# Kernel tuning notes

Hardware: AMD Instinct MI355X
Metric: run time of the kernel (lower is better)

## Reference

```python
import jax, jax.numpy as jnp
import numpy as np

B, N = 2, 200
IMG = 2048
NC = 4                    # node concepts ('Is*')
NODE_CH = NC * 256        # 1024
EC = 3                    # edge concepts minus 'HigherPri'
AC = 4                    # actions
BBOX_MAX = 1024.0
E = N * (N - 1)

# static fully-connected directed edge list (src=i, dst=j, i!=j), row-major order
_ii, _jj = np.meshgrid(np.arange(N), np.arange(N), indexing='ij')
_m = _ii != _jj
SRC = jnp.asarray(_ii[_m])
DST = jnp.asarray(_jj[_m])


def _lin(k, fin, fout):
    kw, kb = jax.random.split(k)
    s = 1.0 / np.sqrt(fin)
    return (jax.random.uniform(kw, (fin, fout), jnp.float32, -s, s),
            jax.random.uniform(kb, (fout,), jnp.float32, -s, s))


def setup_inputs():
    ks = jax.random.split(jax.random.key(0), 16)
    p = {}
    p['roi_features'] = jax.random.normal(ks[0], (B, N, IMG), jnp.float32)
    p['batch_bboxes'] = jax.random.uniform(ks[1], (B, N, 4), jnp.float32) * BBOX_MAX
    p['batch_directions'] = jax.random.normal(ks[2], (B, N, 4), jnp.float32)
    p['batch_priorities'] = jax.random.normal(ks[3], (B, N), jnp.float32)
    p['w1'], p['b1'] = _lin(ks[4], IMG, 512)
    p['w2'], p['b2'] = _lin(ks[5], 512, 256)
    p['w3'], p['b3'] = _lin(ks[6], 256, NODE_CH)
    p['wi'], p['bi'] = _lin(ks[7], NODE_CH, NC)
    p['we1'], p['be1'] = _lin(ks[8], 16, 256)
    p['we2'], p['be2'] = _lin(ks[9], 256, 64)
    p['we3'], p['be3'] = _lin(ks[10], 64, EC)
    p['wp1'], p['bp1'] = _lin(ks[11], EC + 1, 128)
    p['wp2'], p['bp2'] = _lin(ks[12], 128, NODE_CH * AC)
    p['root_w'], _ = _lin(ks[13], NODE_CH, AC)
    _, p['root_b'] = _lin(ks[14], NODE_CH, AC)
    return p


def reference(roi_features, batch_bboxes, batch_directions, batch_priorities,
              w1, b1, w2, b2, w3, b3, wi, bi,
              we1, be1, we2, be2, we3, be3,
              wp1, bp1, wp2, bp2, root_w, root_b):
    # node concept embedding MLP: [B,N,IMG] -> [B,N,NODE_CH]
    h = jax.nn.relu(roi_features @ w1 + b1)
    h = jax.nn.relu(h @ w2 + b2)
    node_concepts = h @ w3 + b3
    node_concepts_explicit = jax.nn.sigmoid(node_concepts @ wi + bi)

    # pairwise attributes for all directed edges (same ordering as torch masks)
    node_attr = jnp.concatenate([batch_bboxes / BBOX_MAX, batch_directions], -1)  # [B,N,8]
    pair = jnp.concatenate([node_attr[:, SRC], node_attr[:, DST]], -1)            # [B,E,16]
    eh = jax.nn.relu(pair @ we1 + be1)
    eh = jax.nn.relu(eh @ we2 + be2)
    edge_attributes = jax.nn.sigmoid(eh @ we3 + be3)                              # [B,E,EC]
    higher_pri = (batch_priorities[:, SRC] > batch_priorities[:, DST]).astype(jnp.float32)
    edge_attributes = jnp.concatenate([edge_attributes, higher_pri[..., None]], -1)  # [B,E,EC+1]

    # NNConv on graph 0: per-edge weight matrix, gather-matmul-scatter
    x = node_concepts[0]                 # [N, NODE_CH]
    e = edge_attributes[0]               # [E, EC+1]
    w = jax.nn.relu(e @ wp1 + bp1) @ wp2 + bp2
    w = w.reshape(E, NODE_CH, AC)        # [E, NODE_CH, AC]
    msg = jnp.einsum('ei,eio->eo', x[SRC], w)          # [E, AC]
    agg = jax.ops.segment_sum(msg, DST, num_segments=N)  # [N, AC]
    next_actions = agg + x @ root_w + root_b
    return (next_actions, node_concepts_explicit[0], edge_attributes[0])
```

## Files before the change

kernel.cpp:

```cpp
#include <hip/hip_runtime.h>
#include <math.h>

#define NN 200
#define ETOT 39800

typedef float float4v __attribute__((ext_vector_type(4)));
typedef short short8 __attribute__((ext_vector_type(8)));
typedef unsigned int uint4v __attribute__((ext_vector_type(4)));

__device__ __forceinline__ float sigf(float x) { return 1.0f / (1.0f + expf(-x)); }

__device__ __forceinline__ unsigned short f2b(float f) {
  unsigned u = __float_as_uint(f);
  u += 0x7fffu + ((u >> 16) & 1u);
  return (unsigned short)(u >> 16);
}
__device__ __forceinline__ float b2f16(unsigned short u) {
  return __uint_as_float(((unsigned)u) << 16);
}
__device__ __forceinline__ unsigned pkbf(float a, float b) {
  return (unsigned)f2b(a) | ((unsigned)f2b(b) << 16);
}

__global__ __launch_bounds__(256) void k_prep(
    const float* __restrict__ w1, const float* __restrict__ w2, const float* __restrict__ w3,
    const float* __restrict__ wp2, const float* __restrict__ we2,
    const float* __restrict__ bbox, const float* __restrict__ dir,
    const float* __restrict__ we1, const float* __restrict__ be1,
    const float* __restrict__ roi, const float* __restrict__ wp1,
    unsigned short* __restrict__ w1T, unsigned short* __restrict__ w2T,
    unsigned short* __restrict__ w3T, unsigned short* __restrict__ WrT,
    unsigned short* __restrict__ we2T, unsigned short* __restrict__ roiB,
    float* __restrict__ P, float* __restrict__ Q, float* __restrict__ wp1T) {
  __shared__ float lds[64][65];
  const int b = blockIdx.x, tid = threadIdx.x;

  if (b < 352) {
    const float* Wf;
    unsigned short* Wt;
    int K, N, t;
    if (b < 256) { Wf = w1; Wt = w1T; K = 2048; N = 512; t = b; }
    else if (b < 288) { Wf = w2; Wt = w2T; K = 512; N = 256; t = b - 256; }
    else { Wf = w3; Wt = w3T; K = 256; N = 1024; t = b - 288; }
    const int K64 = K >> 6;
    const int kt = t % K64, nt = t / K64;
#pragma unroll 4
    for (int i = 0; i < 16; ++i) {
      int idx = tid + i * 256;
      int r = idx >> 6, c = idx & 63;
      lds[r][c] = Wf[(size_t)(kt * 64 + r) * N + nt * 64 + c];
    }
    __syncthreads();
#pragma unroll 4
    for (int i = 0; i < 16; ++i) {
      int idx = tid + i * 256;
      int r = idx >> 6, c = idx & 63;
      Wt[(size_t)(nt * 64 + r) * K + kt * 64 + c] = f2b(lds[c][r]);
    }
  } else if (b < 480) {
    int k = b - 352;
    int o = tid >> 6, l = tid & 63;
    const float* src = wp2 + (size_t)k * 4096;
    unsigned short* dst = WrT + (size_t)(k * 4 + o) * 1024;
    for (int i = l; i < 1024; i += 64) dst[i] = f2b(src[i * 4 + o]);
  } else if (b < 496) {
    int f = (b - 480) * 256 + tid;
    int c = f >> 6, k0 = (f & 63) * 4;
#pragma unroll
    for (int q = 0; q < 4; ++q)
      we2T[c * 256 + k0 + q] = f2b(we2[(k0 + q) * 64 + c]);
  } else if (b < 696) {
    int n = b - 496, c = tid;
    float a[8];
#pragma unroll
    for (int r = 0; r < 4; ++r) a[r] = bbox[n * 4 + r] * (1.0f / 1024.0f);
#pragma unroll
    for (int r = 0; r < 4; ++r) a[4 + r] = dir[n * 4 + r];
    float p = be1[c], q = 0.0f;
#pragma unroll
    for (int r = 0; r < 8; ++r) {
      p += a[r] * we1[r * 256 + c];
      q += a[r] * we1[(8 + r) * 256 + c];
    }
    P[n * 256 + c] = p;
    Q[n * 256 + c] = q;
  } else if (b < 896) {
    int n = b - 696;
    const float4v* R4 = (const float4v*)(roi + (size_t)n * 2048);
    unsigned long long* O = (unsigned long long*)(roiB + (size_t)n * 2048);
#pragma unroll
    for (int j = 0; j < 2; ++j) {
      int idx = tid + j * 256;
      float4v v = R4[idx];
      union { unsigned short us[4]; unsigned long long ll; } pk;
#pragma unroll
      for (int q = 0; q < 4; ++q) pk.us[q] = f2b(v[q]);
      O[idx] = pk.ll;
    }
  } else {
    if (tid < 128) {
      float4v v = {wp1[tid], wp1[128 + tid], wp1[256 + tid], wp1[384 + tid]};
      ((float4v*)wp1T)[tid] = v;
    }
  }
}

template <int KSTEPS, int RELU, int OUTF32, int HASBIAS>
__global__ __launch_bounds__(256) void gemm_mf(const unsigned short* __restrict__ A,
                                               const unsigned short* __restrict__ B,
                                               const float* __restrict__ bias,
                                               void* __restrict__ Cout, int N) {
  constexpr int K = KSTEPS * 128;
  const int tid = threadIdx.x, lane = tid & 63, wv = tid >> 6;
  const int m0 = blockIdx.x * 16, n0 = blockIdx.y * 16;
  const int mr = lane & 15, quad = lane >> 4;
  const unsigned short* Ap = A + (size_t)(m0 + mr) * K + wv * (KSTEPS * 32) + quad * 8;
  const unsigned short* Bp = B + (size_t)(n0 + mr) * K + wv * (KSTEPS * 32) + quad * 8;
  float4v acc = {0.f, 0.f, 0.f, 0.f};
#pragma unroll
  for (int s = 0; s < KSTEPS; ++s) {
    short8 af = *(const short8*)(Ap + s * 32);
    short8 bf = *(const short8*)(Bp + s * 32);
    acc = __builtin_amdgcn_mfma_f32_16x16x32_bf16(af, bf, acc, 0, 0, 0);
  }
  __shared__ float red[4][16][17];
#pragma unroll
  for (int r = 0; r < 4; ++r) red[wv][quad * 4 + r][mr] = acc[r];
  __syncthreads();
  const int row = tid >> 4, col = tid & 15;
  float v = red[0][row][col] + red[1][row][col] + red[2][row][col] + red[3][row][col];
  if (HASBIAS) v += bias[n0 + col];
  if (RELU) v = fmaxf(v, 0.f);
  if (OUTF32)
    ((float*)Cout)[(size_t)(m0 + row) * N + n0 + col] = v;
  else
    ((unsigned short*)Cout)[(size_t)(m0 + row) * N + n0 + col] = f2b(v);
}

__global__ __launch_bounds__(256) void k_nodevec(const unsigned short* __restrict__ xB,
                                                 const float* __restrict__ wi, const float* __restrict__ bi,
                                                 const float* __restrict__ root_w, const float* __restrict__ root_b,
                                                 const float* __restrict__ bp2,
                                                 float* __restrict__ out_nce, float* __restrict__ U,
                                                 float* __restrict__ out0) {
  const int n = blockIdx.x, tid = threadIdx.x;
  float s[12] = {};
#pragma unroll
  for (int i = 0; i < 4; ++i) {
    int k = tid + i * 256;
    float xv = b2f16(xB[n * 1024 + k]);
    float4v wi4 = ((const float4v*)wi)[k];
    float4v rw4 = ((const float4v*)root_w)[k];
    float4v bp4 = ((const float4v*)bp2)[k];
#pragma unroll
    for (int c = 0; c < 4; ++c) {
      s[c] += xv * wi4[c];
      s[4 + c] += xv * rw4[c];
      s[8 + c] += xv * bp4[c];
    }
  }
  __shared__ float part[4][12];
  const int lane = tid & 63, wv = tid >> 6;
#pragma unroll
  for (int r = 0; r < 12; ++r) {
    float v = s[r];
#pragma unroll
    for (int off = 32; off > 0; off >>= 1) v += __shfl_down(v, off, 64);
    if (lane == 0) part[wv][r] = v;
  }
  __syncthreads();
  if (tid < 12) {
    float v = part[0][tid] + part[1][tid] + part[2][tid] + part[3][tid];
    int kind = tid >> 2, c = tid & 3;
    if (kind == 0) out_nce[n * 4 + c] = sigf(v + bi[c]);
    else if (kind == 1) out0[n * 4 + c] = v + root_b[c];
    else U[n * 4 + c] = v;
  }
}

__global__ __launch_bounds__(256) void k_edge(
    const float* __restrict__ P, const float* __restrict__ Q,
    const unsigned short* __restrict__ we2T,
    const float* __restrict__ be2, const float* __restrict__ we3, const float* __restrict__ be3,
    const float* __restrict__ wp1T, const float* __restrict__ bp1,
    const float* __restrict__ pri,
    const float* __restrict__ T, const float* __restrict__ U,
    float* __restrict__ out0, float* __restrict__ out_ea) {
  __shared__ int src_s[64], dst_s[64];
  __shared__ float ea_s[64][4];
  __shared__ float4v wp1s[128];
  __shared__ float bp1s[128];
  __shared__ float4v Ts[2][128];
  __shared__ float Us[2][4];

  const int tid = threadIdx.x;
  const int e0 = blockIdx.x * 64;
  const int s_lo = e0 / 199;

  if (tid < 64) {
    int e = e0 + tid;
    int i = -1, j = 0;
    if (e < ETOT) {
      i = e / 199;
      int jj = e - i * 199;
      j = jj + (jj >= i ? 1 : 0);
    }
    src_s[tid] = i;
    dst_s[tid] = j;
  }
  if (tid < 128) {
    wp1s[tid] = ((const float4v*)wp1T)[tid];
    bp1s[tid] = bp1[tid];
  }
  {
    int row = tid >> 7, c = tid & 127;
    Ts[row][c] = ((const float4v*)T)[(s_lo + row) * 128 + c];
  }
  if (tid < 8) {
    int s = min(s_lo + (tid >> 2), 199);
    Us[tid >> 2][tid & 3] = U[s * 4 + (tid & 3)];
  }
  __syncthreads();

  const int lane = tid & 63;
  const int wv = tid >> 6;
  const int m = lane & 15;
  const int quad = lane >> 4;
  const int eloc = wv * 16 + m;
  const int si = src_s[eloc];
  const int dj = dst_s[eloc];

  float4v acc[4];
#pragma unroll
  for (int ct = 0; ct < 4; ++ct) { acc[ct][0] = 0.f; acc[ct][1] = 0.f; acc[ct][2] = 0.f; acc[ct][3] = 0.f; }

  const short8* W8 = (const short8*)we2T;

  for (int ks = 0; ks < 8; ++ks) {
    union { short8 s; uint4v u; } af;
    af.s = (short8)0;
    if (si >= 0) {
      const float4v* p4 = (const float4v*)(P + si * 256 + ks * 32 + quad * 8);
      const float4v* q4 = (const float4v*)(Q + dj * 256 + ks * 32 + quad * 8);
      float4v v0 = p4[0] + q4[0];
      float4v v1 = p4[1] + q4[1];
      af.u[0] = pkbf(fmaxf(v0[0], 0.f), fmaxf(v0[1], 0.f));
      af.u[1] = pkbf(fmaxf(v0[2], 0.f), fmaxf(v0[3], 0.f));
      af.u[2] = pkbf(fmaxf(v1[0], 0.f), fmaxf(v1[1], 0.f));
      af.u[3] = pkbf(fmaxf(v1[2], 0.f), fmaxf(v1[3], 0.f));
    }
#pragma unroll
    for (int ct = 0; ct < 4; ++ct) {
      short8 bf = W8[(ct * 16 + m) * 32 + ks * 4 + quad];
      acc[ct] = __builtin_amdgcn_mfma_f32_16x16x32_bf16(af.s, bf, acc[ct], 0, 0, 0);
    }
  }

  float ev[4][3];
#pragma unroll
  for (int r = 0; r < 4; ++r) { ev[r][0] = 0.f; ev[r][1] = 0.f; ev[r][2] = 0.f; }
#pragma unroll
  for (int ct = 0; ct < 4; ++ct) {
    const int col = ct * 16 + m;
    const float b2v = be2[col];
    const float w0 = we3[col * 3 + 0], w1v = we3[col * 3 + 1], w2v = we3[col * 3 + 2];
#pragma unroll
    for (int r = 0; r < 4; ++r) {
      float e2 = fmaxf(acc[ct][r] + b2v, 0.f);
      ev[r][0] += e2 * w0;
      ev[r][1] += e2 * w1v;
      ev[r][2] += e2 * w2v;
    }
  }
#pragma unroll
  for (int r = 0; r < 4; ++r)
#pragma unroll
    for (int p = 0; p < 3; ++p) {
      float v = ev[r][p];
      v += __shfl_xor(v, 1, 64);
      v += __shfl_xor(v, 2, 64);
      v += __shfl_xor(v, 4, 64);
      v += __shfl_xor(v, 8, 64);
      ev[r][p] = v;
    }
  if (m == 0) {
#pragma unroll
    for (int r = 0; r < 4; ++r) {
      int el = wv * 16 + quad * 4 + r;
      int ss = src_s[el], dd = dst_s[el];
      if (ss >= 0) {
        float4v o;
        o[0] = sigf(ev[r][0] + be3[0]);
        o[1] = sigf(ev[r][1] + be3[1]);
        o[2] = sigf(ev[r][2] + be3[2]);
        o[3] = (pri[ss] > pri[dd]) ? 1.0f : 0.0f;
        *(float4v*)&ea_s[el][0] = o;
        *(float4v*)(out_ea + (size_t)(e0 + el) * 4) = o;
      }
    }
  }
  __syncthreads();

  const int ee = tid >> 2, pp = tid & 3;
  const int s2 = src_s[ee], d2 = dst_s[ee];
  float4v pm = {0.f, 0.f, 0.f, 0.f};
  if (s2 >= 0) {
    const int srow = s2 - s_lo;
    const float c0 = ea_s[ee][0], c1 = ea_s[ee][1], c2 = ea_s[ee][2], c3 = ea_s[ee][3];
#pragma unroll 8
    for (int t = pp; t < 128; t += 4) {
      float4v w4 = wp1s[t];
      float hv = bp1s[t] + c0 * w4[0] + c1 * w4[1] + c2 * w4[2] + c3 * w4[3];
      hv = fmaxf(hv, 0.f);
      pm += hv * Ts[srow][t];
    }
  }
#pragma unroll
  for (int o = 0; o < 4; ++o) {
    float v = pm[o];
    v += __shfl_xor(v, 1, 64);
    v += __shfl_xor(v, 2, 64);
    pm[o] = v;
  }
  if (s2 >= 0) atomicAdd(&out0[d2 * 4 + pp], Us[s2 - s_lo][pp] + pm[pp]);
}

extern "C" void kernel_launch(void* const* d_in, const int* in_sizes, int n_in,
                              void* d_out, int out_size, void* d_ws, size_t ws_size,
                              hipStream_t stream) {
  (void)in_sizes; (void)n_in; (void)out_size; (void)ws_size;
  const float* roi   = (const float*)d_in[0];
  const float* bbox  = (const float*)d_in[1];
  const float* dir   = (const float*)d_in[2];
  const float* pri   = (const float*)d_in[3];
  const float* w1    = (const float*)d_in[4];
  const float* b1    = (const float*)d_in[5];
  const float* w2    = (const float*)d_in[6];
  const float* b2    = (const float*)d_in[7];
  const float* w3    = (const float*)d_in[8];
  const float* b3    = (const float*)d_in[9];
  const float* wi    = (const float*)d_in[10];
  const float* bi    = (const float*)d_in[11];
  const float* we1   = (const float*)d_in[12];
  const float* be1   = (const float*)d_in[13];
  const float* we2   = (const float*)d_in[14];
  const float* be2   = (const float*)d_in[15];
  const float* we3   = (const float*)d_in[16];
  const float* be3   = (const float*)d_in[17];
  const float* wp1   = (const float*)d_in[18];
  const float* bp1   = (const float*)d_in[19];
  const float* wp2   = (const float*)d_in[20];
  const float* bp2   = (const float*)d_in[21];
  const float* rootw = (const float*)d_in[22];
  const float* rootb = (const float*)d_in[23];

  float* out0 = (float*)d_out;
  float* out1 = out0 + 800;
  float* out2 = out0 + 1600;

  unsigned short* us = (unsigned short*)d_ws;
  unsigned short* w1T  = us;
  unsigned short* w2T  = us + 1048576;
  unsigned short* w3T  = us + 1179648;
  unsigned short* WrT  = us + 1441792;
  unsigned short* we2T = us + 1966080;
  unsigned short* roiB = us + 1982464;
  unsigned short* h1   = us + 2408448;
  unsigned short* h2   = us + 2514944;
  unsigned short* xB   = us + 2568192;
  float* fb   = (float*)(us + 2781184);
  float* Tm   = fb;
  float* Pm   = fb + 106496;
  float* Qm   = fb + 157696;
  float* Um   = fb + 208896;
  float* wp1T = fb + 209696;

  k_prep<<<897, 256, 0, stream>>>(w1, w2, w3, wp2, we2, bbox, dir, we1, be1, roi, wp1,
                                  w1T, w2T, w3T, WrT, we2T, roiB, Pm, Qm, wp1T);

  gemm_mf<16, 1, 0, 1><<<dim3(13, 32), 256, 0, stream>>>(roiB, w1T, b1, h1, 512);
  gemm_mf<4, 1, 0, 1><<<dim3(13, 16), 256, 0, stream>>>(h1, w2T, b2, h2, 256);
  gemm_mf<2, 0, 0, 1><<<dim3(13, 64), 256, 0, stream>>>(h2, w3T, b3, xB, 1024);

  k_nodevec<<<200, 256, 0, stream>>>(xB, wi, bi, rootw, rootb, bp2, out1, Um, out0);

  gemm_mf<8, 0, 1, 0><<<dim3(13, 32), 256, 0, stream>>>(xB, WrT, nullptr, Tm, 512);

  k_edge<<<622, 256, 0, stream>>>(Pm, Qm, we2T, be2, we3, be3, wp1T, bp1, pri, Tm, Um, out0, out2);
}
```

Before: 157.2 us.

## Fuse GEMM chain, nodevec and edge kernels into persistent kernel with grid barriers

Replaces six separate kernel launches with one persistent 512-block kernel that loops over tiles for each stage and separates stages with atomic-counter grid barriers. It also runs the Wr GEMM and the node-vector reductions in the same phase. The aim is to remove per-launch overhead and the inter-kernel drain gaps. In exchange it relies on all 512 blocks being co-resident, or the barriers deadlock, and it adds barrier spin cost plus extra syncthreads inside each tile.

Result: slower. 600.8 us (+282.3%).

```diff
diff --git a/kernel.cpp b/kernel.cpp
--- a/kernel.cpp
+++ b/kernel.cpp
@@ -6,7 +6,6 @@
 
 typedef float float4v __attribute__((ext_vector_type(4)));
 typedef short short8 __attribute__((ext_vector_type(8)));
-typedef unsigned int uint4v __attribute__((ext_vector_type(4)));
 
 __device__ __forceinline__ float sigf(float x) { return 1.0f / (1.0f + expf(-x)); }
 
@@ -18,8 +17,18 @@
 __device__ __forceinline__ float b2f16(unsigned short u) {
   return __uint_as_float(((unsigned)u) << 16);
 }
-__device__ __forceinline__ unsigned pkbf(float a, float b) {
-  return (unsigned)f2b(a) | ((unsigned)f2b(b) << 16);
+
+__device__ __forceinline__ void gbar(unsigned* c, unsigned target) {
+  __threadfence();
+  __syncthreads();
+  if (threadIdx.x == 0) {
+    __hip_atomic_fetch_add(c, 1u, __ATOMIC_ACQ_REL, __HIP_MEMORY_SCOPE_AGENT);
+    while (__hip_atomic_load(c, __ATOMIC_ACQUIRE, __HIP_MEMORY_SCOPE_AGENT) < target) {
+      __builtin_amdgcn_s_sleep(2);
+    }
+  }
+  __syncthreads();
+  __threadfence();
 }
 
 __global__ __launch_bounds__(256) void k_prep(
@@ -31,7 +40,8 @@
     unsigned short* __restrict__ w1T, unsigned short* __restrict__ w2T,
     unsigned short* __restrict__ w3T, unsigned short* __restrict__ WrT,
     unsigned short* __restrict__ we2T, unsigned short* __restrict__ roiB,
-    float* __restrict__ P, float* __restrict__ Q, float* __restrict__ wp1T) {
+    float* __restrict__ P, float* __restrict__ Q, float* __restrict__ wp1T,
+    unsigned* __restrict__ barr) {
   __shared__ float lds[64][65];
   const int b = blockIdx.x, tid = threadIdx.x;
 
@@ -101,18 +111,23 @@
     if (tid < 128) {
       float4v v = {wp1[tid], wp1[128 + tid], wp1[256 + tid], wp1[384 + tid]};
       ((float4v*)wp1T)[tid] = v;
-    }
-  }
-}
+    } else if (tid < 136) {
+      barr[tid - 128] = 0u;
+    }
+  }
+}
+
 
 template <int KSTEPS, int RELU, int OUTF32, int HASBIAS>
-__global__ __launch_bounds__(256) void gemm_mf(const unsigned short* __restrict__ A,
-                                               const unsigned short* __restrict__ B,
-                                               const float* __restrict__ bias,
-                                               void* __restrict__ Cout, int N) {
+__device__ __forceinline__ void gemm_tile(char* sm, int t,
+                                          const unsigned short* __restrict__ A,
+                                          const unsigned short* __restrict__ B,
+                                          const float* __restrict__ bias,
+                                          void* __restrict__ Cout, int N) {
+  float (*red)[16][17] = (float (*)[16][17])sm;
   constexpr int K = KSTEPS * 128;
   const int tid = threadIdx.x, lane = tid & 63, wv = tid >> 6;
-  const int m0 = blockIdx.x * 16, n0 = blockIdx.y * 16;
+  const int m0 = (t % 13) * 16, n0 = (t / 13) * 16;
   const int mr = lane & 15, quad = lane >> 4;
   const unsigned short* Ap = A + (size_t)(m0 + mr) * K + wv * (KSTEPS * 32) + quad * 8;
   const unsigned short* Bp = B + (size_t)(n0 + mr) * K + wv * (KSTEPS * 32) + quad * 8;
@@ -123,7 +138,7 @@
     short8 bf = *(const short8*)(Bp + s * 32);
     acc = __builtin_amdgcn_mfma_f32_16x16x32_bf16(af, bf, acc, 0, 0, 0);
   }
-  __shared__ float red[4][16][17];
+  __syncthreads();
 #pragma unroll
   for (int r = 0; r < 4; ++r) red[wv][quad * 4 + r][mr] = acc[r];
   __syncthreads();
@@ -137,13 +152,15 @@
     ((unsigned short*)Cout)[(size_t)(m0 + row) * N + n0 + col] = f2b(v);
 }
 
-__global__ __launch_bounds__(256) void k_nodevec(const unsigned short* __restrict__ xB,
-                                                 const float* __restrict__ wi, const float* __restrict__ bi,
-                                                 const float* __restrict__ root_w, const float* __restrict__ root_b,
-                                                 const float* __restrict__ bp2,
-                                                 float* __restrict__ out_nce, float* __restrict__ U,
-                                                 float* __restrict__ out0) {
-  const int n = blockIdx.x, tid = threadIdx.x;
+__device__ __forceinline__ void nodevec_task(char* sm, int n,
+                                             const unsigned short* __restrict__ xB,
+                                             const float* __restrict__ wi, const float* __restrict__ bi,
+                                             const float* __restrict__ root_w, const float* __restrict__ root_b,
+                                             const float* __restrict__ bp2,
+                                             float* __restrict__ out_nce, float* __restrict__ U,
+                                             float* __restrict__ out0) {
+  float (*part)[12] = (float (*)[12])sm;
+  const int tid = threadIdx.x;
   float s[12] = {};
 #pragma unroll
   for (int i = 0; i < 4; ++i) {
@@ -159,8 +176,8 @@
       s[8 + c] += xv * bp4[c];
     }
   }
-  __shared__ float part[4][12];
   const int lane = tid & 63, wv = tid >> 6;
+  __syncthreads();
 #pragma unroll
   for (int r = 0; r < 12; ++r) {
     float v = s[r];
@@ -178,24 +195,26 @@
   }
 }
 
-__global__ __launch_bounds__(256) void k_edge(
-    const float* __restrict__ P, const float* __restrict__ Q,
-    const unsigned short* __restrict__ we2T,
-    const float* __restrict__ be2, const float* __restrict__ we3, const float* __restrict__ be3,
-    const float* __restrict__ wp1T, const float* __restrict__ bp1,
-    const float* __restrict__ pri,
-    const float* __restrict__ T, const float* __restrict__ U,
-    float* __restrict__ out0, float* __restrict__ out_ea) {
-  __shared__ int src_s[64], dst_s[64];
-  __shared__ float ea_s[64][4];
-  __shared__ float4v wp1s[128];
-  __shared__ float bp1s[128];
-  __shared__ float4v Ts[2][128];
-  __shared__ float Us[2][4];
+__device__ __forceinline__ void edge_task(char* sm, int t,
+                                          const float* __restrict__ P, const float* __restrict__ Q,
+                                          const unsigned short* __restrict__ we2T,
+                                          const float* __restrict__ be2, const float* __restrict__ we3,
+                                          const float* __restrict__ be3, const float* __restrict__ pri,
+                                          const float* __restrict__ T, const float* __restrict__ U,
+                                          float* __restrict__ out0, float* __restrict__ out_ea) {
+  float4v* wp1s = (float4v*)sm;
+  float* bp1s = (float*)(sm + 2048);
+  float4v (*Ts)[128] = (float4v (*)[128])(sm + 2560);
+  float (*Us)[4] = (float (*)[4])(sm + 6656);
+  int* src_s = (int*)(sm + 6688);
+  int* dst_s = (int*)(sm + 6944);
+  float (*ea_s)[4] = (float (*)[4])(sm + 7200);
 
   const int tid = threadIdx.x;
-  const int e0 = blockIdx.x * 64;
+  const int e0 = t * 64;
   const int s_lo = e0 / 199;
+
+  __syncthreads();
 
   if (tid < 64) {
     int e = e0 + tid;
@@ -208,10 +227,6 @@
     src_s[tid] = i;
     dst_s[tid] = j;
   }
-  if (tid < 128) {
-    wp1s[tid] = ((const float4v*)wp1T)[tid];
-    bp1s[tid] = bp1[tid];
-  }
   {
     int row = tid >> 7, c = tid & 127;
     Ts[row][c] = ((const float4v*)T)[(s_lo + row) * 128 + c];
@@ -237,17 +252,17 @@
   const short8* W8 = (const short8*)we2T;
 
   for (int ks = 0; ks < 8; ++ks) {
-    union { short8 s; uint4v u; } af;
+    union { short8 s; unsigned u[4]; } af;
     af.s = (short8)0;
     if (si >= 0) {
       const float4v* p4 = (const float4v*)(P + si * 256 + ks * 32 + quad * 8);
       const float4v* q4 = (const float4v*)(Q + dj * 256 + ks * 32 + quad * 8);
       float4v v0 = p4[0] + q4[0];
       float4v v1 = p4[1] + q4[1];
-      af.u[0] = pkbf(fmaxf(v0[0], 0.f), fmaxf(v0[1], 0.f));
-      af.u[1] = pkbf(fmaxf(v0[2], 0.f), fmaxf(v0[3], 0.f));
-      af.u[2] = pkbf(fmaxf(v1[0], 0.f), fmaxf(v1[1], 0.f));
-      af.u[3] = pkbf(fmaxf(v1[2], 0.f), fmaxf(v1[3], 0.f));
+      af.u[0] = (unsigned)f2b(fmaxf(v0[0], 0.f)) | ((unsigned)f2b(fmaxf(v0[1], 0.f)) << 16);
+      af.u[1] = (unsigned)f2b(fmaxf(v0[2], 0.f)) | ((unsigned)f2b(fmaxf(v0[3], 0.f)) << 16);
+      af.u[2] = (unsigned)f2b(fmaxf(v1[0], 0.f)) | ((unsigned)f2b(fmaxf(v1[1], 0.f)) << 16);
+      af.u[3] = (unsigned)f2b(fmaxf(v1[2], 0.f)) | ((unsigned)f2b(fmaxf(v1[3], 0.f)) << 16);
     }
 #pragma unroll
     for (int ct = 0; ct < 4; ++ct) {
@@ -308,11 +323,11 @@
     const int srow = s2 - s_lo;
     const float c0 = ea_s[ee][0], c1 = ea_s[ee][1], c2 = ea_s[ee][2], c3 = ea_s[ee][3];
 #pragma unroll 8
-    for (int t = pp; t < 128; t += 4) {
-      float4v w4 = wp1s[t];
-      float hv = bp1s[t] + c0 * w4[0] + c1 * w4[1] + c2 * w4[2] + c3 * w4[3];
+    for (int tt = pp; tt < 128; tt += 4) {
+      float4v w4 = wp1s[tt];
+      float hv = bp1s[tt] + c0 * w4[0] + c1 * w4[1] + c2 * w4[2] + c3 * w4[3];
       hv = fmaxf(hv, 0.f);
-      pm += hv * Ts[srow][t];
+      pm += hv * Ts[srow][tt];
     }
   }
 #pragma unroll
@@ -323,6 +338,51 @@
     pm[o] = v;
   }
   if (s2 >= 0) atomicAdd(&out0[d2 * 4 + pp], Us[s2 - s_lo][pp] + pm[pp]);
+}
+
+__global__ __launch_bounds__(256, 2) void mega(
+    const unsigned short* roiB, const unsigned short* w1T, const float* b1, unsigned short* h1,
+    const unsigned short* w2T, const float* b2, unsigned short* h2,
+    const unsigned short* w3T, const float* b3, unsigned short* xB,
+    const unsigned short* WrT, float* Tm,
+    const float* wi, const float* bi, const float* rootw, const float* rootb, const float* bp2,
+    float* out1, float* Um, float* out0,
+    const float* Pm, const float* Qm, const unsigned short* we2T,
+    const float* be2, const float* we3, const float* be3,
+    const float* wp1T, const float* bp1, const float* pri,
+    float* out2, unsigned* barr) {
+  __shared__ __align__(16) char sm[8448];
+  const int tid = threadIdx.x;
+  const unsigned NB = gridDim.x;
+
+  for (unsigned t = blockIdx.x; t < 416; t += NB)
+    gemm_tile<16, 1, 0, 1>(sm, t, roiB, w1T, b1, h1, 512);
+  gbar(barr + 0, NB);
+
+  for (unsigned t = blockIdx.x; t < 208; t += NB)
+    gemm_tile<4, 1, 0, 1>(sm, t, h1, w2T, b2, h2, 256);
+  gbar(barr + 1, NB);
+
+  for (unsigned t = blockIdx.x; t < 832; t += NB)
+    gemm_tile<2, 0, 0, 1>(sm, t, h2, w3T, b3, xB, 1024);
+  gbar(barr + 2, NB);
+
+  for (unsigned t = blockIdx.x; t < 616; t += NB) {
+    if (t < 416) gemm_tile<8, 0, 1, 0>(sm, t, xB, WrT, nullptr, Tm, 512);
+    else nodevec_task(sm, t - 416, xB, wi, bi, rootw, rootb, bp2, out1, Um, out0);
+  }
+  gbar(barr + 3, NB);
+
+  {
+    float4v* wp1s = (float4v*)sm;
+    float* bp1s = (float*)(sm + 2048);
+    if (tid < 128) {
+      wp1s[tid] = ((const float4v*)wp1T)[tid];
+      bp1s[tid] = bp1[tid];
+    }
+  }
+  for (unsigned t = blockIdx.x; t < 622; t += NB)
+    edge_task(sm, t, Pm, Qm, we2T, be2, we3, be3, pri, Tm, Um, out0, out2);
 }
 
 extern "C" void kernel_launch(void* const* d_in, const int* in_sizes, int n_in,
@@ -374,17 +434,12 @@
   float* Qm   = fb + 157696;
   float* Um   = fb + 208896;
   float* wp1T = fb + 209696;
+  unsigned* barr = (unsigned*)(fb + 210208);
 
   k_prep<<<897, 256, 0, stream>>>(w1, w2, w3, wp2, we2, bbox, dir, we1, be1, roi, wp1,
-                                  w1T, w2T, w3T, WrT, we2T, roiB, Pm, Qm, wp1T);
-
-  gemm_mf<16, 1, 0, 1><<<dim3(13, 32), 256, 0, stream>>>(roiB, w1T, b1, h1, 512);
-  gemm_mf<4, 1, 0, 1><<<dim3(13, 16), 256, 0, stream>>>(h1, w2T, b2, h2, 256);
-  gemm_mf<2, 0, 0, 1><<<dim3(13, 64), 256, 0, stream>>>(h2, w3T, b3, xB, 1024);
-
-  k_nodevec<<<200, 256, 0, stream>>>(xB, wi, bi, rootw, rootb, bp2, out1, Um, out0);
-
-  gemm_mf<8, 0, 1, 0><<<dim3(13, 32), 256, 0, stream>>>(xB, WrT, nullptr, Tm, 512);
-
-  k_edge<<<622, 256, 0, stream>>>(Pm, Qm, we2T, be2, we3, be3, wp1T, bp1, pri, Tm, Um, out0, out2);
-}
+                                  w1T, w2T, w3T, WrT, we2T, roiB, Pm, Qm, wp1T, barr);
+
+  mega<<<512, 256, 0, stream>>>(roiB, w1T, b1, h1, w2T, b2, h2, w3T, b3, xB, WrT, Tm,
+                                wi, bi, rootw, rootb, bp2, out1, Um, out0,
+                                Pm, Qm, we2T, be2, we3, be3, wp1T, bp1, pri, out2, barr);
+}
```

## Fuse node MLP, node-vector and root GEMM chain into one persistent kernel

Applied to the files above, without the earlier changes.

Replaces the three MLP GEMM launches, the node-vector reduction and the Wr GEMM with a single kernel. It uses 13 blocks of 1024 threads, each owning 16 node rows and keeping the intermediate activations h1, h2 and x in shared memory. This removes four kernel launches, their inter-kernel gaps and the global round trips for intermediates. In exchange, only 13 CUs do all the GEMM work, and each block streams the full weight matrices by itself, so per-CU bandwidth and MFMA throughput may become the bottleneck.

Measured after the change: 249.7 us. +58.9%, slower.

```diff
diff --git a/kernel.cpp b/kernel.cpp
--- a/kernel.cpp
+++ b/kernel.cpp
@@ -6,7 +6,6 @@
 
 typedef float float4v __attribute__((ext_vector_type(4)));
 typedef short short8 __attribute__((ext_vector_type(8)));
-typedef unsigned int uint4v __attribute__((ext_vector_type(4)));
 
 __device__ __forceinline__ float sigf(float x) { return 1.0f / (1.0f + expf(-x)); }
 
@@ -17,9 +16,6 @@
 }
 __device__ __forceinline__ float b2f16(unsigned short u) {
   return __uint_as_float(((unsigned)u) << 16);
-}
-__device__ __forceinline__ unsigned pkbf(float a, float b) {
-  return (unsigned)f2b(a) | ((unsigned)f2b(b) << 16);
 }
 
 __global__ __launch_bounds__(256) void k_prep(
@@ -105,76 +101,149 @@
   }
 }
 
-template <int KSTEPS, int RELU, int OUTF32, int HASBIAS>
-__global__ __launch_bounds__(256) void gemm_mf(const unsigned short* __restrict__ A,
-                                               const unsigned short* __restrict__ B,
-                                               const float* __restrict__ bias,
-                                               void* __restrict__ Cout, int N) {
-  constexpr int K = KSTEPS * 128;
-  const int tid = threadIdx.x, lane = tid & 63, wv = tid >> 6;
-  const int m0 = blockIdx.x * 16, n0 = blockIdx.y * 16;
+__global__ __launch_bounds__(1024, 1) void k_chain(
+    const unsigned short* __restrict__ roiB,
+    const unsigned short* __restrict__ w1T, const float* __restrict__ b1,
+    const unsigned short* __restrict__ w2T, const float* __restrict__ b2,
+    const unsigned short* __restrict__ w3T, const float* __restrict__ b3,
+    const unsigned short* __restrict__ WrT,
+    const float* __restrict__ wi, const float* __restrict__ bi,
+    const float* __restrict__ rootw, const float* __restrict__ rootb,
+    const float* __restrict__ bp2,
+    float* __restrict__ out1, float* __restrict__ Um, float* __restrict__ out0,
+    float* __restrict__ Tm) {
+  __shared__ __align__(16) char sm[49664];
+  unsigned short* bufA = (unsigned short*)sm;
+  unsigned short* h1s  = (unsigned short*)(sm + 33024);
+  unsigned short* h2s  = (unsigned short*)sm;
+  unsigned short* xs   = (unsigned short*)(sm + 8448);
+
+  const int tid = threadIdx.x;
+  const int lane = tid & 63, wv = tid >> 6;
+  const int m0 = blockIdx.x * 16;
   const int mr = lane & 15, quad = lane >> 4;
-  const unsigned short* Ap = A + (size_t)(m0 + mr) * K + wv * (KSTEPS * 32) + quad * 8;
-  const unsigned short* Bp = B + (size_t)(n0 + mr) * K + wv * (KSTEPS * 32) + quad * 8;
-  float4v acc = {0.f, 0.f, 0.f, 0.f};
-#pragma unroll
-  for (int s = 0; s < KSTEPS; ++s) {
-    short8 af = *(const short8*)(Ap + s * 32);
-    short8 bf = *(const short8*)(Bp + s * 32);
-    acc = __builtin_amdgcn_mfma_f32_16x16x32_bf16(af, bf, acc, 0, 0, 0);
-  }
-  __shared__ float red[4][16][17];
-#pragma unroll
-  for (int r = 0; r < 4; ++r) red[wv][quad * 4 + r][mr] = acc[r];
+
+  float4v accA[2];
+#pragma unroll
+  for (int ct = 0; ct < 2; ++ct) { accA[ct][0]=0.f; accA[ct][1]=0.f; accA[ct][2]=0.f; accA[ct][3]=0.f; }
+  for (int h = 0; h < 2; ++h) {
+    __syncthreads();
+    for (int i = tid; i < 2048; i += 1024) {
+      int row = i >> 7, off = (i & 127) * 8;
+      *(short8*)(bufA + row * 1032 + off) =
+          *(const short8*)(roiB + (size_t)(m0 + row) * 2048 + h * 1024 + off);
+    }
+    __syncthreads();
+    for (int ks = 0; ks < 32; ++ks) {
+      short8 af = *(const short8*)(bufA + mr * 1032 + ks * 32 + quad * 8);
+#pragma unroll
+      for (int ct = 0; ct < 2; ++ct) {
+        int n = wv * 32 + ct * 16 + mr;
+        short8 bf = *(const short8*)(w1T + (size_t)n * 2048 + h * 1024 + ks * 32 + quad * 8);
+        accA[ct] = __builtin_amdgcn_mfma_f32_16x16x32_bf16(af, bf, accA[ct], 0, 0, 0);
+      }
+    }
+  }
+#pragma unroll
+  for (int ct = 0; ct < 2; ++ct) {
+    int col = wv * 32 + ct * 16 + mr;
+    float bv = b1[col];
+#pragma unroll
+    for (int r = 0; r < 4; ++r)
+      h1s[(quad * 4 + r) * 520 + col] = f2b(fmaxf(accA[ct][r] + bv, 0.f));
+  }
   __syncthreads();
-  const int row = tid >> 4, col = tid & 15;
-  float v = red[0][row][col] + red[1][row][col] + red[2][row][col] + red[3][row][col];
-  if (HASBIAS) v += bias[n0 + col];
-  if (RELU) v = fmaxf(v, 0.f);
-  if (OUTF32)
-    ((float*)Cout)[(size_t)(m0 + row) * N + n0 + col] = v;
-  else
-    ((unsigned short*)Cout)[(size_t)(m0 + row) * N + n0 + col] = f2b(v);
-}
-
-__global__ __launch_bounds__(256) void k_nodevec(const unsigned short* __restrict__ xB,
-                                                 const float* __restrict__ wi, const float* __restrict__ bi,
-                                                 const float* __restrict__ root_w, const float* __restrict__ root_b,
-                                                 const float* __restrict__ bp2,
-                                                 float* __restrict__ out_nce, float* __restrict__ U,
-                                                 float* __restrict__ out0) {
-  const int n = blockIdx.x, tid = threadIdx.x;
-  float s[12] = {};
-#pragma unroll
-  for (int i = 0; i < 4; ++i) {
-    int k = tid + i * 256;
-    float xv = b2f16(xB[n * 1024 + k]);
-    float4v wi4 = ((const float4v*)wi)[k];
-    float4v rw4 = ((const float4v*)root_w)[k];
-    float4v bp4 = ((const float4v*)bp2)[k];
-#pragma unroll
-    for (int c = 0; c < 4; ++c) {
-      s[c] += xv * wi4[c];
-      s[4 + c] += xv * rw4[c];
-      s[8 + c] += xv * bp4[c];
-    }
-  }
-  __shared__ float part[4][12];
-  const int lane = tid & 63, wv = tid >> 6;
-#pragma unroll
-  for (int r = 0; r < 12; ++r) {
-    float v = s[r];
-#pragma unroll
-    for (int off = 32; off > 0; off >>= 1) v += __shfl_down(v, off, 64);
-    if (lane == 0) part[wv][r] = v;
+
+  float4v accB = {0.f, 0.f, 0.f, 0.f};
+  {
+    int n = wv * 16 + mr;
+    for (int ks = 0; ks < 16; ++ks) {
+      short8 af = *(const short8*)(h1s + mr * 520 + ks * 32 + quad * 8);
+      short8 bf = *(const short8*)(w2T + (size_t)n * 512 + ks * 32 + quad * 8);
+      accB = __builtin_amdgcn_mfma_f32_16x16x32_bf16(af, bf, accB, 0, 0, 0);
+    }
+    int col = wv * 16 + mr;
+    float bv = b2[col];
+#pragma unroll
+    for (int r = 0; r < 4; ++r)
+      h2s[(quad * 4 + r) * 264 + col] = f2b(fmaxf(accB[r] + bv, 0.f));
   }
   __syncthreads();
-  if (tid < 12) {
-    float v = part[0][tid] + part[1][tid] + part[2][tid] + part[3][tid];
-    int kind = tid >> 2, c = tid & 3;
-    if (kind == 0) out_nce[n * 4 + c] = sigf(v + bi[c]);
-    else if (kind == 1) out0[n * 4 + c] = v + root_b[c];
-    else U[n * 4 + c] = v;
+
+  float4v accC[4];
+#pragma unroll
+  for (int ct = 0; ct < 4; ++ct) { accC[ct][0]=0.f; accC[ct][1]=0.f; accC[ct][2]=0.f; accC[ct][3]=0.f; }
+  for (int ks = 0; ks < 8; ++ks) {
+    short8 af = *(const short8*)(h2s + mr * 264 + ks * 32 + quad * 8);
+#pragma unroll
+    for (int ct = 0; ct < 4; ++ct) {
+      int n = wv * 64 + ct * 16 + mr;
+      short8 bf = *(const short8*)(w3T + (size_t)n * 256 + ks * 32 + quad * 8);
+      accC[ct] = __builtin_amdgcn_mfma_f32_16x16x32_bf16(af, bf, accC[ct], 0, 0, 0);
+    }
+  }
+#pragma unroll
+  for (int ct = 0; ct < 4; ++ct) {
+    int col = wv * 64 + ct * 16 + mr;
+    float bv = b3[col];
+#pragma unroll
+    for (int r = 0; r < 4; ++r)
+      xs[(quad * 4 + r) * 1032 + col] = f2b(accC[ct][r] + bv);
+  }
+  __syncthreads();
+
+  float4v accD[2];
+#pragma unroll
+  for (int ct = 0; ct < 2; ++ct) { accD[ct][0]=0.f; accD[ct][1]=0.f; accD[ct][2]=0.f; accD[ct][3]=0.f; }
+  for (int ks = 0; ks < 32; ++ks) {
+    short8 af = *(const short8*)(xs + mr * 1032 + ks * 32 + quad * 8);
+#pragma unroll
+    for (int ct = 0; ct < 2; ++ct) {
+      int n = wv * 32 + ct * 16 + mr;
+      short8 bf = *(const short8*)(WrT + (size_t)n * 1024 + ks * 32 + quad * 8);
+      accD[ct] = __builtin_amdgcn_mfma_f32_16x16x32_bf16(af, bf, accD[ct], 0, 0, 0);
+    }
+  }
+#pragma unroll
+  for (int ct = 0; ct < 2; ++ct) {
+    int col = wv * 32 + ct * 16 + mr;
+#pragma unroll
+    for (int r = 0; r < 4; ++r)
+      Tm[(size_t)(m0 + quad * 4 + r) * 512 + col] = accD[ct][r];
+  }
+
+  {
+    int n = m0 + wv;
+    if (n < NN) {
+      float s[12] = {};
+#pragma unroll 4
+      for (int i = 0; i < 16; ++i) {
+        int k = lane + i * 64;
+        float xv = b2f16(xs[wv * 1032 + k]);
+        float4v wi4 = ((const float4v*)wi)[k];
+        float4v rw4 = ((const float4v*)rootw)[k];
+        float4v bp4 = ((const float4v*)bp2)[k];
+#pragma unroll
+        for (int c = 0; c < 4; ++c) {
+          s[c] += xv * wi4[c];
+          s[4 + c] += xv * rw4[c];
+          s[8 + c] += xv * bp4[c];
+        }
+      }
+#pragma unroll
+      for (int r = 0; r < 12; ++r) {
+#pragma unroll
+        for (int off = 32; off > 0; off >>= 1) s[r] += __shfl_down(s[r], off, 64);
+      }
+      if (lane == 0) {
+#pragma unroll
+        for (int c = 0; c < 4; ++c) {
+          out1[n * 4 + c] = sigf(s[c] + bi[c]);
+          out0[n * 4 + c] = s[4 + c] + rootb[c];
+          Um[n * 4 + c] = s[8 + c];
+        }
+      }
+    }
   }
 }
 
@@ -237,17 +306,17 @@
   const short8* W8 = (const short8*)we2T;
 
   for (int ks = 0; ks < 8; ++ks) {
-    union { short8 s; uint4v u; } af;
+    union { short8 s; unsigned u[4]; } af;
     af.s = (short8)0;
     if (si >= 0) {
       const float4v* p4 = (const float4v*)(P + si * 256 + ks * 32 + quad * 8);
       const float4v* q4 = (const float4v*)(Q + dj * 256 + ks * 32 + quad * 8);
       float4v v0 = p4[0] + q4[0];
       float4v v1 = p4[1] + q4[1];
-      af.u[0] = pkbf(fmaxf(v0[0], 0.f), fmaxf(v0[1], 0.f));
-      af.u[1] = pkbf(fmaxf(v0[2], 0.f), fmaxf(v0[3], 0.f));
-      af.u[2] = pkbf(fmaxf(v1[0], 0.f), fmaxf(v1[1], 0.f));
-      af.u[3] = pkbf(fmaxf(v1[2], 0.f), fmaxf(v1[3], 0.f));
+      af.u[0] = (unsigned)f2b(fmaxf(v0[0], 0.f)) | ((unsigned)f2b(fmaxf(v0[1], 0.f)) << 16);
+      af.u[1] = (unsigned)f2b(fmaxf(v0[2], 0.f)) | ((unsigned)f2b(fmaxf(v0[3], 0.f)) << 16);
+      af.u[2] = (unsigned)f2b(fmaxf(v1[0], 0.f)) | ((unsigned)f2b(fmaxf(v1[1], 0.f)) << 16);
+      af.u[3] = (unsigned)f2b(fmaxf(v1[2], 0.f)) | ((unsigned)f2b(fmaxf(v1[3], 0.f)) << 16);
     }
 #pragma unroll
     for (int ct = 0; ct < 4; ++ct) {
@@ -308,11 +377,11 @@
     const int srow = s2 - s_lo;
     const float c0 = ea_s[ee][0], c1 = ea_s[ee][1], c2 = ea_s[ee][2], c3 = ea_s[ee][3];
 #pragma unroll 8
-    for (int t = pp; t < 128; t += 4) {
-      float4v w4 = wp1s[t];
-      float hv = bp1s[t] + c0 * w4[0] + c1 * w4[1] + c2 * w4[2] + c3 * w4[3];
+    for (int tt = pp; tt < 128; tt += 4) {
+      float4v w4 = wp1s[tt];
+      float hv = bp1s[tt] + c0 * w4[0] + c1 * w4[1] + c2 * w4[2] + c3 * w4[3];
       hv = fmaxf(hv, 0.f);
-      pm += hv * Ts[srow][t];
+      pm += hv * Ts[srow][tt];
     }
   }
 #pragma unroll
@@ -365,9 +434,6 @@
   unsigned short* WrT  = us + 1441792;
   unsigned short* we2T = us + 1966080;
   unsigned short* roiB = us + 1982464;
-  unsigned short* h1   = us + 2408448;
-  unsigned short* h2   = us + 2514944;
-  unsigned short* xB   = us + 2568192;
   float* fb   = (float*)(us + 2781184);
   float* Tm   = fb;
   float* Pm   = fb + 106496;
@@ -378,13 +444,8 @@
   k_prep<<<897, 256, 0, stream>>>(w1, w2, w3, wp2, we2, bbox, dir, we1, be1, roi, wp1,
                                   w1T, w2T, w3T, WrT, we2T, roiB, Pm, Qm, wp1T);
 
-  gemm_mf<16, 1, 0, 1><<<dim3(13, 32), 256, 0, stream>>>(roiB, w1T, b1, h1, 512);
-  gemm_mf<4, 1, 0, 1><<<dim3(13, 16), 256, 0, stream>>>(h1, w2T, b2, h2, 256);
-  gemm_mf<2, 0, 0, 1><<<dim3(13, 64), 256, 0, stream>>>(h2, w3T, b3, xB, 1024);
-
-  k_nodevec<<<200, 256, 0, stream>>>(xB, wi, bi, rootw, rootb, bp2, out1, Um, out0);
-
-  gemm_mf<8, 0, 1, 0><<<dim3(13, 32), 256, 0, stream>>>(xB, WrT, nullptr, Tm, 512);
+  k_chain<<<13, 1024, 0, stream>>>(roiB, w1T, b1, w2T, b2, w3T, b3, WrT,
+                                   wi, bi, rootw, rootb, bp2, out1, Um, out0, Tm);
 
   k_edge<<<622, 256, 0, stream>>>(Pm, Qm, we2T, be2, we3, be3, wp1T, bp1, pri, Tm, Um, out0, out2);
 }
```
